# Optimization experiments

Hardware: AMD Instinct MI355X
Metric: run time of the kernel (lower is better)

The kernel has to match this reference:

```python
import jax, jax.numpy as jnp
import numpy as np

G = 7          # num_grid
SG = 12        # size_grid = 84 // 7
A = 18         # predicted_action_space
B = 8192


def _patches(x):
    # x: [B,1,84,84] -> [B, G*G, SG*SG], patch order (i rows, j cols) matching slice_grid loop
    b = x.shape[0]
    x = x.reshape(b, G, SG, G, SG)
    return x.transpose(0, 1, 3, 2, 4).reshape(b, G * G, SG * SG)


def setup_inputs() -> dict:
    key = jax.random.key(0)
    ks = jax.random.split(key, 10)
    last_states = jax.random.uniform(ks[0], (B, 1, 84, 84), jnp.float32) * 255.0
    now_states = jax.random.uniform(ks[1], (B, 1, 84, 84), jnp.float32) * 255.0
    def w(k, shape):
        return jax.random.normal(k, shape, jnp.float32) * 0.05
    return {
        "last_states": last_states,
        "now_states": now_states,
        # mlp_e: 288 -> 256 -> 128 -> 18
        "We1": w(ks[2], (2 * SG * SG, 256)), "be1": jnp.zeros((256,), jnp.float32),
        "We2": w(ks[3], (256, 128)),          "be2": jnp.zeros((128,), jnp.float32),
        "We3": w(ks[4], (128, A)),            "be3": jnp.zeros((A,), jnp.float32),
        # mlp_alpha: 144 -> 64 -> 64 -> 1
        "Wa1": w(ks[5], (SG * SG, 64)), "ba1": jnp.zeros((64,), jnp.float32),
        "Wa2": w(ks[6], (64, 64)),       "ba2": jnp.zeros((64,), jnp.float32),
        "Wa3": w(ks[7], (64, 1)),        "ba3": jnp.zeros((1,), jnp.float32),
    }


def reference(last_states, now_states, We1, be1, We2, be2, We3, be3,
              Wa1, ba1, Wa2, ba2, Wa3, ba3):
    last = last_states / 255.0
    now = now_states / 255.0
    p_now = _patches(now)            # [B, P, 144]
    p_last = _patches(last)          # [B, P, 144]

    # alpha: per-patch scalar via small MLP, softmax over patches
    h = jax.nn.relu(jnp.einsum('bpf,fo->bpo', p_now, Wa1) + ba1)
    h = jax.nn.relu(jnp.einsum('bpf,fo->bpo', h, Wa2) + ba2)
    alpha_logits = (jnp.einsum('bpf,fo->bpo', h, Wa3) + ba3)[..., 0]   # [B, P]
    alpha = jax.nn.softmax(alpha_logits, axis=1)

    # e: per-patch action logits from [diff, now]
    e_in = jnp.concatenate([p_now - p_last, p_now], axis=-1)           # [B, P, 288]
    g = jax.nn.relu(jnp.einsum('bpf,fo->bpo', e_in, We1) + be1)
    g = jax.nn.relu(jnp.einsum('bpf,fo->bpo', g, We2) + be2)
    e = jnp.einsum('bpf,fo->bpo', g, We3) + be3                        # [B, P, A]

    predicted_action_log_probs = jax.nn.log_softmax(
        (e * alpha[..., None]).sum(axis=1), axis=1)                    # [B, A]
    predicted_action_log_probs_each = jax.nn.log_softmax(e, axis=2)    # [B, P, A]
    loss_ent = (alpha * jnp.log(alpha)).sum(axis=1).mean()
    return predicted_action_log_probs, loss_ent, predicted_action_log_probs_each
```

## Files before the change

### kernel.cpp

```cpp
#include <hip/hip_runtime.h>
#include <math.h>

#define NPCH 49
#define NA 18
#define NB 8192
#define TOTAL (NB*NPCH)
#define NBLK (TOTAL/64)

typedef __attribute__((ext_vector_type(8))) short bf16x8;
typedef __attribute__((ext_vector_type(4))) float f32x4;

__device__ __forceinline__ unsigned short f2bf(float f) {
    unsigned int u = __float_as_uint(f);
    return (unsigned short)((u + 0x7FFFu + ((u >> 16) & 1u)) >> 16);
}

#define MF(a,b,c) __builtin_amdgcn_mfma_f32_16x16x32_bf16((a),(b),(c),0,0,0)
#define RAWBAR() do { \
    asm volatile("s_waitcnt lgkmcnt(0)" ::: "memory"); \
    __builtin_amdgcn_s_barrier(); \
    asm volatile("" ::: "memory"); \
} while (0)

#define WS_US (256*512)

__global__ __launch_bounds__(256)
void prep_weights(const float* __restrict__ We1, const float* __restrict__ We2,
                  const float* __restrict__ We3, const float* __restrict__ Wa1,
                  const float* __restrict__ Wa2, unsigned short* __restrict__ wst)
{
    int i = blockIdx.x * 256 + threadIdx.x;
    if (i >= WS_US) return;
    const int fs = i >> 9, l = (i >> 3) & 63, j = i & 7;
    const int kh = ((l >> 4) << 3) + j;
    const int nl = l & 15;
    float v = 0.0f;
    if (fs < 20) {
        int s = fs >> 2, w = fs & 3;
        int k = s * 32 + kh, n = w * 16 + nl;
        v = (k < 144) ? Wa1[k * 64 + n] : 0.0f;
    } else if (fs < 28) {
        int q = fs - 20, s = q >> 2, w = q & 3;
        v = Wa2[(s * 32 + kh) * 64 + (w * 16 + nl)];
    } else if (fs < 32) {
        v = 0.0f;
    } else if (fs < 176) {
        int q = fs - 32, s = q >> 4, nt = (q >> 2) & 3, w = q & 3;
        v = We1[(s * 32 + kh) * 256 + (w * 64 + nt * 16 + nl)];
    } else if (fs < 240) {
        int q = fs - 176, s = q >> 3, nt = (q >> 2) & 1, w = q & 3;
        v = We2[(s * 32 + kh) * 128 + (w * 32 + nt * 16 + nl)];
    } else if (fs < 248) {
        int q = fs - 240, s = q >> 1, nt = q & 1;
        int n = nt * 16 + nl;
        v = (n < NA) ? We3[(s * 32 + kh) * NA + n] : 0.0f;
    }
    wst[i] = f2bf(v);
}

__device__ __forceinline__ void wb_frag(unsigned short* base, f32x4 a)
{
    float r0 = fmaxf(a[0], 0.f), r1 = fmaxf(a[1], 0.f);
    float r2 = fmaxf(a[2], 0.f), r3 = fmaxf(a[3], 0.f);
    unsigned u01, u23;
    asm("v_cvt_pk_bf16_f32 %0, %1, %2" : "=v"(u01) : "v"(r0), "v"(r1));
    asm("v_cvt_pk_bf16_f32 %0, %1, %2" : "=v"(u23) : "v"(r2), "v"(r3));
    base[0]  = (unsigned short)u01;
    base[8]  = (unsigned short)(u01 >> 16);
    base[16] = (unsigned short)u23;
    base[24] = (unsigned short)(u23 >> 16);
}

__global__ __launch_bounds__(256, 3)
void fused_mfma_kernel(const float* __restrict__ last_s, const float* __restrict__ now_s,
                       const unsigned short* __restrict__ wstream,
                       const float* __restrict__ be1, const float* __restrict__ be2,
                       const float* __restrict__ be3, const float* __restrict__ ba1,
                       const float* __restrict__ ba2, const float* __restrict__ ba3,
                       const float* __restrict__ Wa3,
                       float* __restrict__ out_each, float* __restrict__ ws_alpha)
{
    __shared__ __align__(16) unsigned char smem[46080];
    unsigned short* Ein = (unsigned short*)smem;
    unsigned short* H1  = (unsigned short*)smem;
    unsigned short* H2  = (unsigned short*)smem;
    unsigned short* HA1 = (unsigned short*)(smem + 36864);
    float*          APT = (float*)(smem + 45056);

    const int t    = threadIdx.x;
    const int lane = t & 63;
    const int wid  = t >> 6;
    const int g    = lane >> 4;
    const int rl   = lane & 15;
    const int row0 = blockIdx.x * 64;

#define GFRAG(fs) (*(const bf16x8*)(wstream + (size_t)(fs) * 512 + lane * 8))

    bf16x8 wa1f[5], wa2f[2];
    #pragma unroll
    for (int s = 0; s < 5; ++s) wa1f[s] = GFRAG(s * 4 + wid);
    #pragma unroll
    for (int s = 0; s < 2; ++s) wa2f[s] = GFRAG(20 + s * 4 + wid);
    bf16x8 wA[4], wB[4], wC[4];
    #pragma unroll
    for (int nt = 0; nt < 4; ++nt) wA[nt] = GFRAG(32 + 0 * 16 + nt * 4 + wid);
    #pragma unroll
    for (int nt = 0; nt < 4; ++nt) wB[nt] = GFRAG(32 + 1 * 16 + nt * 4 + wid);
    #pragma unroll
    for (int nt = 0; nt < 4; ++nt) wC[nt] = GFRAG(32 + 2 * 16 + nt * 4 + wid);

    {
        #pragma unroll
        for (int it = 0; it < 9; ++it) {
            const int idx = t + it * 256;
            const int r   = idx / 36;
            const int q   = idx - r * 36;
            const int R   = row0 + r;
            const int im  = R / 49;
            const int p   = R - im * 49;
            const int pi  = p / 7,  pj  = p - pi * 7;
            const int fr  = q / 3,  fc4 = q - fr * 3;
            const size_t base = (size_t)im * 7056 + (pi * 12 + fr) * 84 + pj * 12 + fc4 * 4;
            const float4 n4 = *(const float4*)(now_s + base);
            const float4 l4 = *(const float4*)(last_s + base);
            const float k255 = 1.0f / 255.0f;
            float d0 = (n4.x - l4.x) * k255, d1 = (n4.y - l4.y) * k255;
            float d2 = (n4.z - l4.z) * k255, d3 = (n4.w - l4.w) * k255;
            float w0 = n4.x * k255, w1 = n4.y * k255;
            float w2 = n4.z * k255, w3 = n4.w * k255;
            unsigned da, db, wa, wb;
            asm("v_cvt_pk_bf16_f32 %0, %1, %2" : "=v"(da) : "v"(d0), "v"(d1));
            asm("v_cvt_pk_bf16_f32 %0, %1, %2" : "=v"(db) : "v"(d2), "v"(d3));
            asm("v_cvt_pk_bf16_f32 %0, %1, %2" : "=v"(wa) : "v"(w0), "v"(w1));
            asm("v_cvt_pk_bf16_f32 %0, %1, %2" : "=v"(wb) : "v"(w2), "v"(w3));
            const int wp = r >> 4, rp = r & 15;
            const int f  = fr * 12 + fc4 * 4;
            const int s1 = f >> 5, g1 = (f >> 3) & 3, j1 = f & 7;
            *(uint2*)(Ein + (wp * 9 + s1) * 512 + g1 * 128 + rp * 8 + j1) = (uint2){da, db};
            const int k2 = 144 + f;
            const int s2 = k2 >> 5, g2 = (k2 >> 3) & 3, j2 = k2 & 7;
            *(uint2*)(Ein + (wp * 9 + s2) * 512 + g2 * 128 + rp * 8 + j2) = (uint2){wa, wb};
        }
    }
    RAWBAR();

    const int colA = wid * 16 + rl;
    {
        const float b1 = ba1[colA];
        f32x4 accA[4];
        #pragma unroll
        for (int mt = 0; mt < 4; ++mt) accA[mt] = (f32x4){b1, b1, b1, b1};
        #pragma unroll
        for (int sa = 0; sa < 5; ++sa) {
            int ok = 144 + sa * 32 + g * 8;
            if (ok > 280) ok = 280;
            #pragma unroll
            for (int mt = 0; mt < 4; ++mt) {
                const bf16x8 af = *(const bf16x8*)(Ein + (mt * 9 + (ok >> 5)) * 512 +
                                                   ((ok >> 3) & 3) * 128 + rl * 8);
                accA[mt] = MF(af, wa1f[sa], accA[mt]);
            }
        }
        const int sA  = wid >> 1;
        const int hiA = (wid & 1) * 2 + (rl >> 3);
        const int jA  = rl & 7;
        #pragma unroll
        for (int mt = 0; mt < 4; ++mt)
            wb_frag(HA1 + (mt * 2 + sA) * 512 + hiA * 128 + g * 32 + jA, accA[mt]);
    }

    f32x4 acc1[4][4];
    #pragma unroll
    for (int nt = 0; nt < 4; ++nt) {
        const float b = be1[wid * 64 + nt * 16 + rl];
        #pragma unroll
        for (int mt = 0; mt < 4; ++mt) acc1[mt][nt] = (f32x4){b, b, b, b};
    }

#define E1_STEP(W, s, sn) do { \
    const bf16x8 x0_ = *(const bf16x8*)(Ein + (0 * 9 + (s)) * 512 + lane * 8); \
    const bf16x8 x1_ = *(const bf16x8*)(Ein + (1 * 9 + (s)) * 512 + lane * 8); \
    const bf16x8 x2_ = *(const bf16x8*)(Ein + (2 * 9 + (s)) * 512 + lane * 8); \
    const bf16x8 x3_ = *(const bf16x8*)(Ein + (3 * 9 + (s)) * 512 + lane * 8); \
    _Pragma("unroll") \
    for (int nt = 0; nt < 4; ++nt) { \
        acc1[0][nt] = MF(x0_, W[nt], acc1[0][nt]); \
        acc1[1][nt] = MF(x1_, W[nt], acc1[1][nt]); \
        acc1[2][nt] = MF(x2_, W[nt], acc1[2][nt]); \
        acc1[3][nt] = MF(x3_, W[nt], acc1[3][nt]); \
    } \
    if ((sn) <= 8) { \
        _Pragma("unroll") \
        for (int nt = 0; nt < 4; ++nt) W[nt] = GFRAG(32 + (sn) * 16 + nt * 4 + wid); \
    } \
} while (0)

    E1_STEP(wA, 0, 3); E1_STEP(wB, 1, 4); E1_STEP(wC, 2, 5);
    E1_STEP(wA, 3, 6); E1_STEP(wB, 4, 7);

    RAWBAR();

    {
        const float b2 = ba2[colA];
        const float w3 = Wa3[colA];
        f32x4 accB[4];
        #pragma unroll
        for (int mt = 0; mt < 4; ++mt) accB[mt] = (f32x4){b2, b2, b2, b2};
        #pragma unroll
        for (int s = 0; s < 2; ++s) {
            #pragma unroll
            for (int mt = 0; mt < 4; ++mt) {
                const bf16x8 af = *(const bf16x8*)(HA1 + (mt * 2 + s) * 512 + lane * 8);
                accB[mt] = MF(af, wa2f[s], accB[mt]);
            }
        }
        #pragma unroll
        for (int mt = 0; mt < 4; ++mt) {
            #pragma unroll
            for (int r = 0; r < 4; ++r) {
                float v = fmaxf(accB[mt][r], 0.0f) * w3;
                v += __shfl_xor(v, 1); v += __shfl_xor(v, 2);
                v += __shfl_xor(v, 4); v += __shfl_xor(v, 8);
                if (rl == 0) APT[wid * 64 + mt * 16 + g * 4 + r] = v;
            }
        }
    }

    E1_STEP(wC, 5, 8); E1_STEP(wA, 6, 9); E1_STEP(wB, 7, 9); E1_STEP(wC, 8, 9);
#undef E1_STEP

    bf16x8 vA[2], vB[2], vC[2];
    #pragma unroll
    for (int nt = 0; nt < 2; ++nt) vA[nt] = GFRAG(176 + 0 * 8 + nt * 4 + wid);
    #pragma unroll
    for (int nt = 0; nt < 2; ++nt) vB[nt] = GFRAG(176 + 1 * 8 + nt * 4 + wid);
    #pragma unroll
    for (int nt = 0; nt < 2; ++nt) vC[nt] = GFRAG(176 + 2 * 8 + nt * 4 + wid);

    RAWBAR();

    if (t < 64)
        ws_alpha[row0 + t] = APT[t] + APT[64 + t] + APT[128 + t] + APT[192 + t] + ba3[0];

    #pragma unroll
    for (int mt = 0; mt < 4; ++mt) {
        #pragma unroll
        for (int nt = 0; nt < 4; ++nt) {
            const int col = wid * 64 + nt * 16 + rl;
            wb_frag(H1 + (mt * 8 + (col >> 5)) * 512 + ((col >> 3) & 3) * 128 +
                    g * 32 + (col & 7), acc1[mt][nt]);
        }
    }
    RAWBAR();

    f32x4 acc2[4][2];
    #pragma unroll
    for (int nt = 0; nt < 2; ++nt) {
        const float b = be2[wid * 32 + nt * 16 + rl];
        #pragma unroll
        for (int mt = 0; mt < 4; ++mt) acc2[mt][nt] = (f32x4){b, b, b, b};
    }

#define E2_STEP(V, s2, sn) do { \
    const bf16x8 x0_ = *(const bf16x8*)(H1 + (0 * 8 + (s2)) * 512 + lane * 8); \
    const bf16x8 x1_ = *(const bf16x8*)(H1 + (1 * 8 + (s2)) * 512 + lane * 8); \
    const bf16x8 x2_ = *(const bf16x8*)(H1 + (2 * 8 + (s2)) * 512 + lane * 8); \
    const bf16x8 x3_ = *(const bf16x8*)(H1 + (3 * 8 + (s2)) * 512 + lane * 8); \
    _Pragma("unroll") \
    for (int nt = 0; nt < 2; ++nt) { \
        acc2[0][nt] = MF(x0_, V[nt], acc2[0][nt]); \
        acc2[1][nt] = MF(x1_, V[nt], acc2[1][nt]); \
        acc2[2][nt] = MF(x2_, V[nt], acc2[2][nt]); \
        acc2[3][nt] = MF(x3_, V[nt], acc2[3][nt]); \
    } \
    if ((sn) <= 7) { \
        _Pragma("unroll") \
        for (int nt = 0; nt < 2; ++nt) V[nt] = GFRAG(176 + (sn) * 8 + nt * 4 + wid); \
    } \
} while (0)

    E2_STEP(vA, 0, 3); E2_STEP(vB, 1, 4); E2_STEP(vC, 2, 5);
    E2_STEP(vA, 3, 6); E2_STEP(vB, 4, 7); E2_STEP(vC, 5, 8);
    E2_STEP(vA, 6, 8); E2_STEP(vB, 7, 8);
#undef E2_STEP

    bf16x8 w3f[8];
    #pragma unroll
    for (int q = 0; q < 8; ++q) w3f[q] = GFRAG(240 + q);

    RAWBAR();

    #pragma unroll
    for (int mt = 0; mt < 4; ++mt) {
        #pragma unroll
        for (int nt = 0; nt < 2; ++nt) {
            const int c2 = nt * 16 + rl;
            wb_frag(H2 + (mt * 4 + wid) * 512 + ((c2 >> 3) & 3) * 128 +
                    g * 32 + (c2 & 7), acc2[mt][nt]);
        }
    }
    RAWBAR();

    {
        f32x4 acc3[2];
        #pragma unroll
        for (int nt = 0; nt < 2; ++nt) {
            const int col = nt * 16 + rl;
            const float b = (col < NA) ? be3[col] : 0.0f;
            acc3[nt] = (f32x4){b, b, b, b};
        }
        #pragma unroll
        for (int s = 0; s < 4; ++s) {
            const bf16x8 af = *(const bf16x8*)(H2 + (wid * 4 + s) * 512 + lane * 8);
            acc3[0] = MF(af, w3f[s * 2 + 0], acc3[0]);
            acc3[1] = MF(af, w3f[s * 2 + 1], acc3[1]);
        }
        const bool v1 = (rl < 2);
        #pragma unroll
        for (int r = 0; r < 4; ++r) {
            const int prow = row0 + wid * 16 + g * 4 + r;
            float x0 = acc3[0][r];
            float x1 = acc3[1][r];
            float m = fmaxf(x0, v1 ? x1 : -3.0e38f);
            m = fmaxf(m, __shfl_xor(m, 1)); m = fmaxf(m, __shfl_xor(m, 2));
            m = fmaxf(m, __shfl_xor(m, 4)); m = fmaxf(m, __shfl_xor(m, 8));
            float sm = expf(x0 - m) + (v1 ? expf(x1 - m) : 0.0f);
            sm += __shfl_xor(sm, 1); sm += __shfl_xor(sm, 2);
            sm += __shfl_xor(sm, 4); sm += __shfl_xor(sm, 8);
            const float L = m + logf(sm);
            float* o = out_each + (size_t)prow * NA;
            o[rl] = x0 - L;
            if (v1) o[16 + rl] = x1 - L;
        }
    }
#undef GFRAG
}

__global__ __launch_bounds__(64)
void alpha_combine_kernel(const float* __restrict__ ws_alpha,
                          const float* __restrict__ out_each,
                          float* __restrict__ out_probs,
                          float* __restrict__ ws_ent)
{
    const int b = blockIdx.x;
    const int lane = threadIdx.x;

    float lg = (lane < NPCH) ? ws_alpha[b * NPCH + lane] : -3.0e38f;
    float m = lg;
    #pragma unroll
    for (int off = 32; off > 0; off >>= 1) m = fmaxf(m, __shfl_xor(m, off, 64));
    float ex = (lane < NPCH) ? expf(lg - m) : 0.0f;
    float s = ex;
    #pragma unroll
    for (int off = 32; off > 0; off >>= 1) s += __shfl_xor(s, off, 64);
    const float ls = logf(s);
    const float alpha = ex / s;

    float ent = (lane < NPCH) ? alpha * (lg - m - ls) : 0.0f;
    #pragma unroll
    for (int off = 32; off > 0; off >>= 1) ent += __shfl_xor(ent, off, 64);
    if (lane == 0) ws_ent[b] = ent;

    float acc = 0.0f;
    const float* eb = out_each + (size_t)b * NPCH * NA;
    for (int p = 0; p < NPCH; ++p) {
        const float ap = __shfl(alpha, p, 64);
        if (lane < NA) acc += ap * eb[p * NA + lane];
    }
    float mm = (lane < NA) ? acc : -3.0e38f;
    #pragma unroll
    for (int off = 32; off > 0; off >>= 1) mm = fmaxf(mm, __shfl_xor(mm, off, 64));
    float ee = (lane < NA) ? expf(acc - mm) : 0.0f;
    #pragma unroll
    for (int off = 32; off > 0; off >>= 1) ee += __shfl_xor(ee, off, 64);
    if (lane < NA) out_probs[b * NA + lane] = acc - mm - logf(ee);
}

__global__ __launch_bounds__(256)
void ent_reduce_kernel(const float* __restrict__ ws_ent, float* __restrict__ out_scalar)
{
    float s = 0.0f;
    for (int i = threadIdx.x; i < NB; i += 256) s += ws_ent[i];
    #pragma unroll
    for (int off = 32; off > 0; off >>= 1) s += __shfl_xor(s, off, 64);
    __shared__ float ps[4];
    if ((threadIdx.x & 63) == 0) ps[threadIdx.x >> 6] = s;
    __syncthreads();
    if (threadIdx.x == 0)
        out_scalar[0] = (ps[0] + ps[1] + ps[2] + ps[3]) * (1.0f / NB);
}

extern "C" void kernel_launch(void* const* d_in, const int* in_sizes, int n_in,
                              void* d_out, int out_size, void* d_ws, size_t ws_size,
                              hipStream_t stream)
{
    (void)in_sizes; (void)n_in; (void)out_size; (void)ws_size;

    const float* last_s = (const float*)d_in[0];
    const float* now_s  = (const float*)d_in[1];
    const float* We1 = (const float*)d_in[2];  const float* be1 = (const float*)d_in[3];
    const float* We2 = (const float*)d_in[4];  const float* be2 = (const float*)d_in[5];
    const float* We3 = (const float*)d_in[6];  const float* be3 = (const float*)d_in[7];
    const float* Wa1 = (const float*)d_in[8];  const float* ba1 = (const float*)d_in[9];
    const float* Wa2 = (const float*)d_in[10]; const float* ba2 = (const float*)d_in[11];
    const float* Wa3 = (const float*)d_in[12]; const float* ba3 = (const float*)d_in[13];

    float* out = (float*)d_out;
    float* out_probs = out;
    float* out_ent   = out + NB * NA;
    float* out_each  = out + NB * NA + 1;

    float* ws_alpha = (float*)d_ws;
    float* ws_ent   = ws_alpha + TOTAL;
    unsigned short* wst = (unsigned short*)(ws_ent + NB);

    prep_weights<<<dim3((WS_US + 255) / 256), dim3(256), 0, stream>>>(
        We1, We2, We3, Wa1, Wa2, wst);

    fused_mfma_kernel<<<dim3(NBLK), dim3(256), 0, stream>>>(
        last_s, now_s, wst, be1, be2, be3, ba1, ba2, ba3, Wa3,
        out_each, ws_alpha);

    alpha_combine_kernel<<<dim3(NB), dim3(64), 0, stream>>>(
        ws_alpha, out_each, out_probs, ws_ent);

    ent_reduce_kernel<<<dim3(1), dim3(256), 0, stream>>>(ws_ent, out_ent);
}
```

Measured before the change: 227.5 us.

## Split fused MLP kernel work across eight waves per block instead of four

Doubles the block to 512 threads and splits the layer-1 and layer-2 output columns of the e-MLP across eight waves, so each wave holds half as many accumulators and weight fragments. The alpha MLP and the final layer still run on only four waves, and the other four wait at barriers. The goal is lower register pressure per wave and more waves in flight to hide latency. In exchange, weight fragments are loaded by more waves, four waves sit idle during the alpha and final-layer phases, and barrier cost rises with the larger block.

```diff
diff --git a/kernel.cpp b/kernel.cpp
--- a/kernel.cpp
+++ b/kernel.cpp
@@ -71,7 +71,7 @@
     base[24] = (unsigned short)(u23 >> 16);
 }
 
-__global__ __launch_bounds__(256, 3)
+__global__ __launch_bounds__(512, 6)
 void fused_mfma_kernel(const float* __restrict__ last_s, const float* __restrict__ now_s,
                        const unsigned short* __restrict__ wstream,
                        const float* __restrict__ be1, const float* __restrict__ be2,
@@ -89,63 +89,67 @@
 
     const int t    = threadIdx.x;
     const int lane = t & 63;
-    const int wid  = t >> 6;
+    const int W    = t >> 6;
     const int g    = lane >> 4;
     const int rl   = lane & 15;
     const int row0 = blockIdx.x * 64;
 
 #define GFRAG(fs) (*(const bf16x8*)(wstream + (size_t)(fs) * 512 + lane * 8))
+#define E1FS(s, gidx) (32 + (s) * 16 + (((gidx) & 3) << 2) + ((gidx) >> 2))
+#define E2FS(s) (176 + (s) * 8 + ((W & 1) << 2) + (W >> 1))
 
     bf16x8 wa1f[5], wa2f[2];
-    #pragma unroll
-    for (int s = 0; s < 5; ++s) wa1f[s] = GFRAG(s * 4 + wid);
-    #pragma unroll
-    for (int s = 0; s < 2; ++s) wa2f[s] = GFRAG(20 + s * 4 + wid);
-    bf16x8 wA[4], wB[4], wC[4];
-    #pragma unroll
-    for (int nt = 0; nt < 4; ++nt) wA[nt] = GFRAG(32 + 0 * 16 + nt * 4 + wid);
-    #pragma unroll
-    for (int nt = 0; nt < 4; ++nt) wB[nt] = GFRAG(32 + 1 * 16 + nt * 4 + wid);
-    #pragma unroll
-    for (int nt = 0; nt < 4; ++nt) wC[nt] = GFRAG(32 + 2 * 16 + nt * 4 + wid);
+    if (W < 4) {
+        #pragma unroll
+        for (int s = 0; s < 5; ++s) wa1f[s] = GFRAG(s * 4 + W);
+        #pragma unroll
+        for (int s = 0; s < 2; ++s) wa2f[s] = GFRAG(20 + s * 4 + W);
+    }
+    const int ga = W * 2, gb = W * 2 + 1;
+    bf16x8 wA[2], wB[2], wC[2];
+    wA[0] = GFRAG(E1FS(0, ga)); wA[1] = GFRAG(E1FS(0, gb));
+    wB[0] = GFRAG(E1FS(1, ga)); wB[1] = GFRAG(E1FS(1, gb));
+    wC[0] = GFRAG(E1FS(2, ga)); wC[1] = GFRAG(E1FS(2, gb));
 
     {
         #pragma unroll
-        for (int it = 0; it < 9; ++it) {
-            const int idx = t + it * 256;
-            const int r   = idx / 36;
-            const int q   = idx - r * 36;
-            const int R   = row0 + r;
-            const int im  = R / 49;
-            const int p   = R - im * 49;
-            const int pi  = p / 7,  pj  = p - pi * 7;
-            const int fr  = q / 3,  fc4 = q - fr * 3;
-            const size_t base = (size_t)im * 7056 + (pi * 12 + fr) * 84 + pj * 12 + fc4 * 4;
-            const float4 n4 = *(const float4*)(now_s + base);
-            const float4 l4 = *(const float4*)(last_s + base);
-            const float k255 = 1.0f / 255.0f;
-            float d0 = (n4.x - l4.x) * k255, d1 = (n4.y - l4.y) * k255;
-            float d2 = (n4.z - l4.z) * k255, d3 = (n4.w - l4.w) * k255;
-            float w0 = n4.x * k255, w1 = n4.y * k255;
-            float w2 = n4.z * k255, w3 = n4.w * k255;
-            unsigned da, db, wa, wb;
-            asm("v_cvt_pk_bf16_f32 %0, %1, %2" : "=v"(da) : "v"(d0), "v"(d1));
-            asm("v_cvt_pk_bf16_f32 %0, %1, %2" : "=v"(db) : "v"(d2), "v"(d3));
-            asm("v_cvt_pk_bf16_f32 %0, %1, %2" : "=v"(wa) : "v"(w0), "v"(w1));
-            asm("v_cvt_pk_bf16_f32 %0, %1, %2" : "=v"(wb) : "v"(w2), "v"(w3));
-            const int wp = r >> 4, rp = r & 15;
-            const int f  = fr * 12 + fc4 * 4;
-            const int s1 = f >> 5, g1 = (f >> 3) & 3, j1 = f & 7;
-            *(uint2*)(Ein + (wp * 9 + s1) * 512 + g1 * 128 + rp * 8 + j1) = (uint2){da, db};
-            const int k2 = 144 + f;
-            const int s2 = k2 >> 5, g2 = (k2 >> 3) & 3, j2 = k2 & 7;
-            *(uint2*)(Ein + (wp * 9 + s2) * 512 + g2 * 128 + rp * 8 + j2) = (uint2){wa, wb};
-        }
-    }
-    RAWBAR();
-
-    const int colA = wid * 16 + rl;
-    {
+        for (int it = 0; it < 5; ++it) {
+            const int idx = t + it * 512;
+            if (idx < 2304) {
+                const int r   = idx / 36;
+                const int q   = idx - r * 36;
+                const int R   = row0 + r;
+                const int im  = R / 49;
+                const int p   = R - im * 49;
+                const int pi  = p / 7,  pj  = p - pi * 7;
+                const int fr  = q / 3,  fc4 = q - fr * 3;
+                const size_t base = (size_t)im * 7056 + (pi * 12 + fr) * 84 + pj * 12 + fc4 * 4;
+                const float4 n4 = *(const float4*)(now_s + base);
+                const float4 l4 = *(const float4*)(last_s + base);
+                const float k255 = 1.0f / 255.0f;
+                float d0 = (n4.x - l4.x) * k255, d1 = (n4.y - l4.y) * k255;
+                float d2 = (n4.z - l4.z) * k255, d3 = (n4.w - l4.w) * k255;
+                float w0 = n4.x * k255, w1 = n4.y * k255;
+                float w2 = n4.z * k255, w3 = n4.w * k255;
+                unsigned da, db, wa, wb;
+                asm("v_cvt_pk_bf16_f32 %0, %1, %2" : "=v"(da) : "v"(d0), "v"(d1));
+                asm("v_cvt_pk_bf16_f32 %0, %1, %2" : "=v"(db) : "v"(d2), "v"(d3));
+                asm("v_cvt_pk_bf16_f32 %0, %1, %2" : "=v"(wa) : "v"(w0), "v"(w1));
+                asm("v_cvt_pk_bf16_f32 %0, %1, %2" : "=v"(wb) : "v"(w2), "v"(w3));
+                const int wp = r >> 4, rp = r & 15;
+                const int f  = fr * 12 + fc4 * 4;
+                const int s1 = f >> 5, g1 = (f >> 3) & 3, j1 = f & 7;
+                *(uint2*)(Ein + (wp * 9 + s1) * 512 + g1 * 128 + rp * 8 + j1) = (uint2){da, db};
+                const int k2 = 144 + f;
+                const int s2 = k2 >> 5, g2 = (k2 >> 3) & 3, j2 = k2 & 7;
+                *(uint2*)(Ein + (wp * 9 + s2) * 512 + g2 * 128 + rp * 8 + j2) = (uint2){wa, wb};
+            }
+        }
+    }
+    RAWBAR();
+
+    const int colA = (W & 3) * 16 + rl;
+    if (W < 4) {
         const float b1 = ba1[colA];
         f32x4 accA[4];
         #pragma unroll
@@ -161,37 +165,37 @@
                 accA[mt] = MF(af, wa1f[sa], accA[mt]);
             }
         }
-        const int sA  = wid >> 1;
-        const int hiA = (wid & 1) * 2 + (rl >> 3);
+        const int sA  = W >> 1;
+        const int hiA = (W & 1) * 2 + (rl >> 3);
         const int jA  = rl & 7;
         #pragma unroll
         for (int mt = 0; mt < 4; ++mt)
             wb_frag(HA1 + (mt * 2 + sA) * 512 + hiA * 128 + g * 32 + jA, accA[mt]);
     }
 
-    f32x4 acc1[4][4];
-    #pragma unroll
-    for (int nt = 0; nt < 4; ++nt) {
-        const float b = be1[wid * 64 + nt * 16 + rl];
+    f32x4 acc1[4][2];
+    #pragma unroll
+    for (int nt = 0; nt < 2; ++nt) {
+        const float b = be1[W * 32 + nt * 16 + rl];
         #pragma unroll
         for (int mt = 0; mt < 4; ++mt) acc1[mt][nt] = (f32x4){b, b, b, b};
     }
 
-#define E1_STEP(W, s, sn) do { \
+#define E1_STEP(Wr, s, sn) do { \
     const bf16x8 x0_ = *(const bf16x8*)(Ein + (0 * 9 + (s)) * 512 + lane * 8); \
     const bf16x8 x1_ = *(const bf16x8*)(Ein + (1 * 9 + (s)) * 512 + lane * 8); \
     const bf16x8 x2_ = *(const bf16x8*)(Ein + (2 * 9 + (s)) * 512 + lane * 8); \
     const bf16x8 x3_ = *(const bf16x8*)(Ein + (3 * 9 + (s)) * 512 + lane * 8); \
     _Pragma("unroll") \
-    for (int nt = 0; nt < 4; ++nt) { \
-        acc1[0][nt] = MF(x0_, W[nt], acc1[0][nt]); \
-        acc1[1][nt] = MF(x1_, W[nt], acc1[1][nt]); \
-        acc1[2][nt] = MF(x2_, W[nt], acc1[2][nt]); \
-        acc1[3][nt] = MF(x3_, W[nt], acc1[3][nt]); \
+    for (int nt = 0; nt < 2; ++nt) { \
+        acc1[0][nt] = MF(x0_, Wr[nt], acc1[0][nt]); \
+        acc1[1][nt] = MF(x1_, Wr[nt], acc1[1][nt]); \
+        acc1[2][nt] = MF(x2_, Wr[nt], acc1[2][nt]); \
+        acc1[3][nt] = MF(x3_, Wr[nt], acc1[3][nt]); \
     } \
     if ((sn) <= 8) { \
-        _Pragma("unroll") \
-        for (int nt = 0; nt < 4; ++nt) W[nt] = GFRAG(32 + (sn) * 16 + nt * 4 + wid); \
+        Wr[0] = GFRAG(E1FS((sn), ga)); \
+        Wr[1] = GFRAG(E1FS((sn), gb)); \
     } \
 } while (0)
 
@@ -200,7 +204,7 @@
 
     RAWBAR();
 
-    {
+    if (W < 4) {
         const float b2 = ba2[colA];
         const float w3 = Wa3[colA];
         f32x4 accB[4];
@@ -221,7 +225,7 @@
                 float v = fmaxf(accB[mt][r], 0.0f) * w3;
                 v += __shfl_xor(v, 1); v += __shfl_xor(v, 2);
                 v += __shfl_xor(v, 4); v += __shfl_xor(v, 8);
-                if (rl == 0) APT[wid * 64 + mt * 16 + g * 4 + r] = v;
+                if (rl == 0) APT[W * 64 + mt * 16 + g * 4 + r] = v;
             }
         }
     }
@@ -229,13 +233,8 @@
     E1_STEP(wC, 5, 8); E1_STEP(wA, 6, 9); E1_STEP(wB, 7, 9); E1_STEP(wC, 8, 9);
 #undef E1_STEP
 
-    bf16x8 vA[2], vB[2], vC[2];
-    #pragma unroll
-    for (int nt = 0; nt < 2; ++nt) vA[nt] = GFRAG(176 + 0 * 8 + nt * 4 + wid);
-    #pragma unroll
-    for (int nt = 0; nt < 2; ++nt) vB[nt] = GFRAG(176 + 1 * 8 + nt * 4 + wid);
-    #pragma unroll
-    for (int nt = 0; nt < 2; ++nt) vC[nt] = GFRAG(176 + 2 * 8 + nt * 4 + wid);
+    bf16x8 vA, vB, vC;
+    vA = GFRAG(E2FS(0)); vB = GFRAG(E2FS(1)); vC = GFRAG(E2FS(2));
 
     RAWBAR();
 
@@ -245,20 +244,19 @@
     #pragma unroll
     for (int mt = 0; mt < 4; ++mt) {
         #pragma unroll
-        for (int nt = 0; nt < 4; ++nt) {
-            const int col = wid * 64 + nt * 16 + rl;
+        for (int nt = 0; nt < 2; ++nt) {
+            const int col = W * 32 + nt * 16 + rl;
             wb_frag(H1 + (mt * 8 + (col >> 5)) * 512 + ((col >> 3) & 3) * 128 +
                     g * 32 + (col & 7), acc1[mt][nt]);
         }
     }
     RAWBAR();
 
-    f32x4 acc2[4][2];
-    #pragma unroll
-    for (int nt = 0; nt < 2; ++nt) {
-        const float b = be2[wid * 32 + nt * 16 + rl];
-        #pragma unroll
-        for (int mt = 0; mt < 4; ++mt) acc2[mt][nt] = (f32x4){b, b, b, b};
+    f32x4 acc2[4];
+    {
+        const float b = be2[W * 16 + rl];
+        #pragma unroll
+        for (int mt = 0; mt < 4; ++mt) acc2[mt] = (f32x4){b, b, b, b};
     }
 
 #define E2_STEP(V, s2, sn) do { \
@@ -266,17 +264,11 @@
     const bf16x8 x1_ = *(const bf16x8*)(H1 + (1 * 8 + (s2)) * 512 + lane * 8); \
     const bf16x8 x2_ = *(const bf16x8*)(H1 + (2 * 8 + (s2)) * 512 + lane * 8); \
     const bf16x8 x3_ = *(const bf16x8*)(H1 + (3 * 8 + (s2)) * 512 + lane * 8); \
-    _Pragma("unroll") \
-    for (int nt = 0; nt < 2; ++nt) { \
-        acc2[0][nt] = MF(x0_, V[nt], acc2[0][nt]); \
-        acc2[1][nt] = MF(x1_, V[nt], acc2[1][nt]); \
-        acc2[2][nt] = MF(x2_, V[nt], acc2[2][nt]); \
-        acc2[3][nt] = MF(x3_, V[nt], acc2[3][nt]); \
-    } \
-    if ((sn) <= 7) { \
-        _Pragma("unroll") \
-        for (int nt = 0; nt < 2; ++nt) V[nt] = GFRAG(176 + (sn) * 8 + nt * 4 + wid); \
-    } \
+    acc2[0] = MF(x0_, V, acc2[0]); \
+    acc2[1] = MF(x1_, V, acc2[1]); \
+    acc2[2] = MF(x2_, V, acc2[2]); \
+    acc2[3] = MF(x3_, V, acc2[3]); \
+    if ((sn) <= 7) V = GFRAG(E2FS(sn)); \
 } while (0)
 
     E2_STEP(vA, 0, 3); E2_STEP(vB, 1, 4); E2_STEP(vC, 2, 5);
@@ -285,23 +277,23 @@
 #undef E2_STEP
 
     bf16x8 w3f[8];
-    #pragma unroll
-    for (int q = 0; q < 8; ++q) w3f[q] = GFRAG(240 + q);
-
-    RAWBAR();
-
-    #pragma unroll
-    for (int mt = 0; mt < 4; ++mt) {
-        #pragma unroll
-        for (int nt = 0; nt < 2; ++nt) {
-            const int c2 = nt * 16 + rl;
-            wb_frag(H2 + (mt * 4 + wid) * 512 + ((c2 >> 3) & 3) * 128 +
-                    g * 32 + (c2 & 7), acc2[mt][nt]);
-        }
-    }
+    if (W < 4) {
+        #pragma unroll
+        for (int q = 0; q < 8; ++q) w3f[q] = GFRAG(240 + q);
+    }
+
     RAWBAR();
 
     {
+        const int c2 = W * 16 + rl;
+        #pragma unroll
+        for (int mt = 0; mt < 4; ++mt)
+            wb_frag(H2 + (mt * 4 + (c2 >> 5)) * 512 + ((c2 >> 3) & 3) * 128 +
+                    g * 32 + (c2 & 7), acc2[mt]);
+    }
+    RAWBAR();
+
+    if (W < 4) {
         f32x4 acc3[2];
         #pragma unroll
         for (int nt = 0; nt < 2; ++nt) {
@@ -311,14 +303,14 @@
         }
         #pragma unroll
         for (int s = 0; s < 4; ++s) {
-            const bf16x8 af = *(const bf16x8*)(H2 + (wid * 4 + s) * 512 + lane * 8);
+            const bf16x8 af = *(const bf16x8*)(H2 + (W * 4 + s) * 512 + lane * 8);
             acc3[0] = MF(af, w3f[s * 2 + 0], acc3[0]);
             acc3[1] = MF(af, w3f[s * 2 + 1], acc3[1]);
         }
         const bool v1 = (rl < 2);
         #pragma unroll
         for (int r = 0; r < 4; ++r) {
-            const int prow = row0 + wid * 16 + g * 4 + r;
+            const int prow = row0 + W * 16 + g * 4 + r;
             float x0 = acc3[0][r];
             float x1 = acc3[1][r];
             float m = fmaxf(x0, v1 ? x1 : -3.0e38f);
@@ -334,6 +326,8 @@
         }
     }
 #undef GFRAG
+#undef E1FS
+#undef E2FS
 }
 
 __global__ __launch_bounds__(64)
@@ -417,7 +411,7 @@
     prep_weights<<<dim3((WS_US + 255) / 256), dim3(256), 0, stream>>>(
         We1, We2, We3, Wa1, Wa2, wst);
 
-    fused_mfma_kernel<<<dim3(NBLK), dim3(256), 0, stream>>>(
+    fused_mfma_kernel<<<dim3(NBLK), dim3(512), 0, stream>>>(
         last_s, now_s, wst, be1, be2, be3, ba1, ba2, ba3, Wa3,
         out_each, ws_alpha);
 
```

Result: slower. 330.5 us (+45.3%).
